# Kernel tuning notes

Hardware: AMD Instinct MI355X
Metric: run time of the kernel (lower is better)

## Reference

```python
import jax, jax.numpy as jnp
import numpy as np

INFEATURES = 4096
OUTFEATURES = 11008
GROUP_SIZE = 128
N_GROUPS = INFEATURES // GROUP_SIZE  # 32
PACK = 8  # 32 bits / 4 bits


def _unpack_int4(packed):
    # packed: [R, C//8] int32 -> [R, C] int32 nibbles in [0, 15]
    shifts = (jnp.arange(PACK, dtype=jnp.int32) * 4)
    nib = (packed[:, :, None] >> shifts[None, None, :]) & 0xF
    return nib.reshape(packed.shape[0], packed.shape[1] * PACK)


def setup_inputs() -> dict:
    key = jax.random.key(0)
    k1, k2, k3, k4, k5 = jax.random.split(key, 5)
    x = jax.random.normal(k1, (2048, INFEATURES), dtype=jnp.float32)
    qweight = jax.random.randint(k2, (INFEATURES, OUTFEATURES // PACK), 0, 2147483647, dtype=jnp.int32)
    qzeros = jax.random.randint(k3, (N_GROUPS, OUTFEATURES // PACK), 0, 2147483647, dtype=jnp.int32)
    scales = jax.random.uniform(k4, (N_GROUPS, OUTFEATURES), minval=0.001, maxval=0.01, dtype=jnp.float32)
    bias = jax.random.normal(k5, (OUTFEATURES,), dtype=jnp.float32) * 0.01
    return {"x": x, "qweight": qweight, "qzeros": qzeros, "scales": scales, "bias": bias}


def reference(x, qweight, qzeros, scales, bias):
    # convert_from_uint4: dequantize packed int4 weight with per-group scale/zero
    w_int = _unpack_int4(qweight)                       # [in, out] int4 values
    z_int = _unpack_int4(qzeros)                        # [n_groups, out]
    dt = scales.dtype
    # broadcast group params to per-row (trivial g_idx: row i -> group i // GROUP_SIZE)
    z = jnp.repeat(z_int.astype(dt), GROUP_SIZE, axis=0)      # [in, out]
    s = jnp.repeat(scales, GROUP_SIZE, axis=0)                # [in, out]
    weight = (w_int.astype(dt) - z) * s                       # [in, out]
    out = jnp.matmul(x, weight) + bias                        # [tokens, out]
    return out
```

## Files before the change

kernel.cpp:

```cpp
#include <hip/hip_runtime.h>

typedef __bf16 bf16_t;
typedef bf16_t bf16x8 __attribute__((ext_vector_type(8)));
typedef float  floatx4 __attribute__((ext_vector_type(4)));
typedef unsigned int uint;

constexpr int Mdim = 2048;
constexpr int Kdim = 4096;
constexpr int Ndim = 11008;
constexpr int NPK  = Ndim / 8;
constexpr int BM = 128, BN = 128, BK = 64;
constexpr int SA = 72;
constexpr int SB = 72;
constexpr int SQ = 68;

#define GLOAD_LDS16(g, l) \
    __builtin_amdgcn_global_load_lds((const __attribute__((address_space(1))) void*)(g), \
                                     (__attribute__((address_space(3))) void*)(l), 16, 0, 0)

__global__ void xcast_kernel(const float* __restrict__ x, bf16_t* __restrict__ xb)
{
    const int i = (blockIdx.x * 256 + threadIdx.x) * 8;
    const float4 a = *(const float4*)(x + i);
    const float4 b = *(const float4*)(x + i + 4);
    bf16x8 v;
    v[0] = (bf16_t)a.x; v[1] = (bf16_t)a.y; v[2] = (bf16_t)a.z; v[3] = (bf16_t)a.w;
    v[4] = (bf16_t)b.x; v[5] = (bf16_t)b.y; v[6] = (bf16_t)b.z; v[7] = (bf16_t)b.w;
    *(bf16x8*)(xb + i) = v;
}

__global__ __launch_bounds__(256, 4)
void wdeq_kernel(const uint* __restrict__ qweight, const uint* __restrict__ qzeros,
                 const float* __restrict__ scales, bf16_t* __restrict__ wt)
{
    __shared__ uint qbuf[16 * SQ];
    const int t  = threadIdx.x;
    const int n0 = blockIdx.x * 128;
    const int k0 = blockIdx.y * 64;
    const int c0 = n0 >> 3;
    const int g  = k0 >> 7;

    const int qk  = t >> 2;
    const int qc4 = (t & 3) * 4;
    const uint4 w4 = *(const uint4*)(qweight + (size_t)(k0 + qk) * NPK + c0 + qc4);
    qbuf[(qc4 + 0) * SQ + qk] = w4.x;
    qbuf[(qc4 + 1) * SQ + qk] = w4.y;
    qbuf[(qc4 + 2) * SQ + qk] = w4.z;
    qbuf[(qc4 + 3) * SQ + qk] = w4.w;
    __syncthreads();

    const int nloc  = t & 127;
    const int khalf = t >> 7;
    const int cc    = nloc >> 3;
    const int jsh   = (nloc & 7) * 4;

    const uint  zw = qzeros[(size_t)g * NPK + c0 + cc];
    const float s  = scales[(size_t)g * Ndim + n0 + nloc];
    const float zs = (float)((zw >> jsh) & 15u) * s;
    const uint* qrow = &qbuf[cc * SQ + khalf * 32];
    bf16_t* dst = wt + (size_t)(n0 + nloc) * Kdim + k0 + khalf * 32;
#pragma unroll
    for (int j = 0; j < 4; ++j) {
        const uint4 qa = *(const uint4*)(qrow + j * 8);
        const uint4 qb = *(const uint4*)(qrow + j * 8 + 4);
        bf16x8 v;
        v[0] = (bf16_t)((float)((qa.x >> jsh) & 15u) * s - zs);
        v[1] = (bf16_t)((float)((qa.y >> jsh) & 15u) * s - zs);
        v[2] = (bf16_t)((float)((qa.z >> jsh) & 15u) * s - zs);
        v[3] = (bf16_t)((float)((qa.w >> jsh) & 15u) * s - zs);
        v[4] = (bf16_t)((float)((qb.x >> jsh) & 15u) * s - zs);
        v[5] = (bf16_t)((float)((qb.y >> jsh) & 15u) * s - zs);
        v[6] = (bf16_t)((float)((qb.z >> jsh) & 15u) * s - zs);
        v[7] = (bf16_t)((float)((qb.w >> jsh) & 15u) * s - zs);
        *(bf16x8*)(dst + j * 8) = v;
    }
}

template <bool PREX>
__global__ __launch_bounds__(256, 4)
void gemm_kernel(const float* __restrict__ x, const bf16_t* __restrict__ xb,
                 const bf16_t* __restrict__ wt, const float* __restrict__ bias,
                 float* __restrict__ out)
{
    constexpr int SAg = PREX ? 64 : 72;
    __shared__ bf16_t As[128 * SAg];
    __shared__ bf16_t Bs[128 * 64];

    const int t    = threadIdx.x;
    const int m0   = blockIdx.y * BM;
    const int n0   = blockIdx.x * BN;
    const int wave = t >> 6;
    const int lane = t & 63;
    const int quad = lane >> 4;
    const int l16  = lane & 15;
    const int mw = (wave >> 1) * 64;
    const int nw = (wave & 1) * 64;

    floatx4 acc[4][4];
#pragma unroll
    for (int i = 0; i < 4; ++i)
#pragma unroll
        for (int j = 0; j < 4; ++j)
            acc[i][j] = (floatx4){0.f, 0.f, 0.f, 0.f};

    const int am = t >> 3;
    const int ao = t & 7;
    const int lr = lane >> 3;
    const int lo = (lane & 7) * 8;

    for (int kt = 0; kt < Kdim / BK; ++kt) {
        const int k0 = kt * BK;

        if (PREX) {
#pragma unroll
            for (int p = 0; p < 4; ++p) {
                const int q = wave * 4 + p;
                GLOAD_LDS16(xb + (size_t)(m0 + q * 8 + lr) * Kdim + k0 + lo,
                            As + q * 512);
            }
        } else {
#pragma unroll
            for (int p = 0; p < 4; ++p) {
                const int m = p * 32 + am;
                const float* src = x + (size_t)(m0 + m) * Kdim + k0 + ao * 8;
                const float4 a = *(const float4*)src;
                const float4 b = *(const float4*)(src + 4);
                bf16x8 v;
                v[0] = (bf16_t)a.x; v[1] = (bf16_t)a.y; v[2] = (bf16_t)a.z; v[3] = (bf16_t)a.w;
                v[4] = (bf16_t)b.x; v[5] = (bf16_t)b.y; v[6] = (bf16_t)b.z; v[7] = (bf16_t)b.w;
                *(bf16x8*)&As[m * SAg + ao * 8] = v;
            }
        }
#pragma unroll
        for (int p = 0; p < 4; ++p) {
            const int q = wave * 4 + p;
            GLOAD_LDS16(wt + (size_t)(n0 + q * 8 + lr) * Kdim + k0 + lo,
                        Bs + q * 512);
        }
        __syncthreads();

#pragma unroll
        for (int s = 0; s < 2; ++s) {
            bf16x8 fa[4], fb[4];
#pragma unroll
            for (int mt = 0; mt < 4; ++mt)
                fa[mt] = *(const bf16x8*)&As[(mw + mt * 16 + l16) * SAg + s * 32 + quad * 8];
#pragma unroll
            for (int nt = 0; nt < 4; ++nt)
                fb[nt] = *(const bf16x8*)&Bs[(nw + nt * 16 + l16) * 64 + s * 32 + quad * 8];
#pragma unroll
            for (int mt = 0; mt < 4; ++mt)
#pragma unroll
                for (int nt = 0; nt < 4; ++nt)
                    acc[mt][nt] = __builtin_amdgcn_mfma_f32_16x16x32_bf16(fa[mt], fb[nt], acc[mt][nt], 0, 0, 0);
        }
        __syncthreads();
    }

#pragma unroll
    for (int nt = 0; nt < 4; ++nt) {
        const int col = n0 + nw + nt * 16 + l16;
        const float b = bias[col];
#pragma unroll
        for (int mt = 0; mt < 4; ++mt) {
#pragma unroll
            for (int r = 0; r < 4; ++r) {
                const int row = m0 + mw + mt * 16 + quad * 4 + r;
                out[(size_t)row * Ndim + col] = acc[mt][nt][r] + b;
            }
        }
    }
}

template <bool PRE>
__global__ __launch_bounds__(256, 3)
void qgemm_kernel(const float* __restrict__ x,
                  const bf16_t* __restrict__ xb,
                  const uint* __restrict__ qweight,
                  const uint* __restrict__ qzeros,
                  const float* __restrict__ scales,
                  const float* __restrict__ bias,
                  float* __restrict__ out)
{
    __shared__ bf16_t As[BM * SA];
    __shared__ bf16_t Bs[BN * SB];
    __shared__ uint   qbuf[16 * SQ];

    const int t  = threadIdx.x;
    const int m0 = blockIdx.y * BM;
    const int n0 = blockIdx.x * BN;
    const int c0 = n0 >> 3;

    const int wave = t >> 6;
    const int lane = t & 63;
    const int quad = lane >> 4;
    const int l16  = lane & 15;
    const int mw = (wave >> 1) * 64;
    const int nw = (wave & 1) * 64;

    floatx4 acc[4][4];
#pragma unroll
    for (int i = 0; i < 4; ++i)
#pragma unroll
        for (int j = 0; j < 4; ++j)
            acc[i][j] = (floatx4){0.f, 0.f, 0.f, 0.f};

    const int am = t >> 3;
    const int ao = t & 7;
    const int qk  = t >> 2;
    const int qc4 = (t & 3) * 4;
    const int nloc  = t & 127;
    const int khalf = t >> 7;
    const int cc    = nloc >> 3;
    const int jsh   = (nloc & 7) * 4;

    for (int kt = 0; kt < Kdim / BK; ++kt) {
        const int k0 = kt * BK;
        const int g  = k0 >> 7;

#pragma unroll
        for (int p = 0; p < 4; ++p) {
            const int m = p * 32 + am;
            if (PRE) {
                const bf16x8 v = *(const bf16x8*)(xb + (size_t)(m0 + m) * Kdim + k0 + ao * 8);
                *(bf16x8*)&As[m * SA + ao * 8] = v;
            } else {
                const float* src = x + (size_t)(m0 + m) * Kdim + k0 + ao * 8;
                const float4 a = *(const float4*)src;
                const float4 b = *(const float4*)(src + 4);
                bf16x8 v;
                v[0] = (bf16_t)a.x; v[1] = (bf16_t)a.y; v[2] = (bf16_t)a.z; v[3] = (bf16_t)a.w;
                v[4] = (bf16_t)b.x; v[5] = (bf16_t)b.y; v[6] = (bf16_t)b.z; v[7] = (bf16_t)b.w;
                *(bf16x8*)&As[m * SA + ao * 8] = v;
            }
        }
        {
            const uint4 w4 = *(const uint4*)(qweight + (size_t)(k0 + qk) * NPK + c0 + qc4);
            qbuf[(qc4 + 0) * SQ + qk] = w4.x;
            qbuf[(qc4 + 1) * SQ + qk] = w4.y;
            qbuf[(qc4 + 2) * SQ + qk] = w4.z;
            qbuf[(qc4 + 3) * SQ + qk] = w4.w;
        }
        __syncthreads();

        {
            const uint  zw = qzeros[(size_t)g * NPK + c0 + cc];
            const float s  = scales[(size_t)g * Ndim + n0 + nloc];
            const float zs = (float)((zw >> jsh) & 15u) * s;
            const uint* qrow = &qbuf[cc * SQ + khalf * 32];
#pragma unroll
            for (int j = 0; j < 4; ++j) {
                const uint4 qa = *(const uint4*)(qrow + j * 8);
                const uint4 qb = *(const uint4*)(qrow + j * 8 + 4);
                bf16x8 v;
                v[0] = (bf16_t)((float)((qa.x >> jsh) & 15u) * s - zs);
                v[1] = (bf16_t)((float)((qa.y >> jsh) & 15u) * s - zs);
                v[2] = (bf16_t)((float)((qa.z >> jsh) & 15u) * s - zs);
                v[3] = (bf16_t)((float)((qa.w >> jsh) & 15u) * s - zs);
                v[4] = (bf16_t)((float)((qb.x >> jsh) & 15u) * s - zs);
                v[5] = (bf16_t)((float)((qb.y >> jsh) & 15u) * s - zs);
                v[6] = (bf16_t)((float)((qb.z >> jsh) & 15u) * s - zs);
                v[7] = (bf16_t)((float)((qb.w >> jsh) & 15u) * s - zs);
                *(bf16x8*)&Bs[nloc * SB + khalf * 32 + j * 8] = v;
            }
        }
        __syncthreads();

#pragma unroll
        for (int s = 0; s < 2; ++s) {
            bf16x8 fa[4], fb[4];
#pragma unroll
            for (int mt = 0; mt < 4; ++mt)
                fa[mt] = *(const bf16x8*)&As[(mw + mt * 16 + l16) * SA + s * 32 + quad * 8];
#pragma unroll
            for (int nt = 0; nt < 4; ++nt)
                fb[nt] = *(const bf16x8*)&Bs[(nw + nt * 16 + l16) * SB + s * 32 + quad * 8];
#pragma unroll
            for (int mt = 0; mt < 4; ++mt)
#pragma unroll
                for (int nt = 0; nt < 4; ++nt)
                    acc[mt][nt] = __builtin_amdgcn_mfma_f32_16x16x32_bf16(fa[mt], fb[nt], acc[mt][nt], 0, 0, 0);
        }
        __syncthreads();
    }

#pragma unroll
    for (int nt = 0; nt < 4; ++nt) {
        const int col = n0 + nw + nt * 16 + l16;
        const float b = bias[col];
#pragma unroll
        for (int mt = 0; mt < 4; ++mt) {
#pragma unroll
            for (int r = 0; r < 4; ++r) {
                const int row = m0 + mw + mt * 16 + quad * 4 + r;
                out[(size_t)row * Ndim + col] = acc[mt][nt][r] + b;
            }
        }
    }
}

extern "C" void kernel_launch(void* const* d_in, const int* in_sizes, int n_in,
                              void* d_out, int out_size, void* d_ws, size_t ws_size,
                              hipStream_t stream)
{
    const float* x        = (const float*)d_in[0];
    const uint*  qweight  = (const uint*)d_in[1];
    const uint*  qzeros   = (const uint*)d_in[2];
    const float* scales   = (const float*)d_in[3];
    const float* bias     = (const float*)d_in[4];
    float*       out      = (float*)d_out;

    const size_t wb_bytes = (size_t)Kdim * Ndim * sizeof(bf16_t);
    const size_t xb_bytes = (size_t)Mdim * Kdim * sizeof(bf16_t);

    dim3 ggrid(Ndim / BN, Mdim / BM);

    if (ws_size >= wb_bytes) {
        bf16_t* wt = (bf16_t*)d_ws;
        wdeq_kernel<<<dim3(Ndim / 128, Kdim / 64), 256, 0, stream>>>(qweight, qzeros, scales, wt);
        if (ws_size >= wb_bytes + xb_bytes) {
            bf16_t* xb = (bf16_t*)((char*)d_ws + wb_bytes);
            xcast_kernel<<<(Mdim * Kdim) / (256 * 8), 256, 0, stream>>>(x, xb);
            gemm_kernel<true><<<ggrid, dim3(256), 0, stream>>>(x, xb, wt, bias, out);
        } else {
            gemm_kernel<false><<<ggrid, dim3(256), 0, stream>>>(x, nullptr, wt, bias, out);
        }
    } else {
        bf16_t* xb = (bf16_t*)d_ws;
        if (ws_size >= xb_bytes) {
            xcast_kernel<<<(Mdim * Kdim) / (256 * 8), 256, 0, stream>>>(x, xb);
            qgemm_kernel<true><<<ggrid, dim3(256), 0, stream>>>(x, xb, qweight, qzeros, scales, bias, out);
        } else {
            qgemm_kernel<false><<<ggrid, dim3(256), 0, stream>>>(x, xb, qweight, qzeros, scales, bias, out);
        }
    }
}
```

Measured before the change: 409.8 us.

## Replace bf16 GEMM with 256x128 double-buffered 8-wave kernel with swizzled LDS

Replaces the 128x128 single-buffered GEMM with a 512-thread kernel computing 256x128 tiles. It double-buffers LDS, prefetches the next K tiles via global_load_lds interleaved with MFMA using explicit waitcnt, barriers and setprio, XOR-swizzles LDS to avoid bank conflicts, and remaps block indices for L2 locality. The goal is to hide global load latency and raise MFMA utilisation. The price is larger LDS use, lower occupancy and hand-tuned wait counts that could be fragile. The old gemm fallback without a cached x cast is dropped.

```diff
diff --git a/kernel.cpp b/kernel.cpp
--- a/kernel.cpp
+++ b/kernel.cpp
@@ -9,14 +9,20 @@
 constexpr int Kdim = 4096;
 constexpr int Ndim = 11008;
 constexpr int NPK  = Ndim / 8;
+constexpr int SQ   = 68;
 constexpr int BM = 128, BN = 128, BK = 64;
-constexpr int SA = 72;
-constexpr int SB = 72;
-constexpr int SQ = 68;
+constexpr int SA = 72, SB = 72;
 
 #define GLOAD_LDS16(g, l) \
     __builtin_amdgcn_global_load_lds((const __attribute__((address_space(1))) void*)(g), \
                                      (__attribute__((address_space(3))) void*)(l), 16, 0, 0)
+#define MFMA(a, b, c) __builtin_amdgcn_mfma_f32_16x16x32_bf16((a), (b), (c), 0, 0, 0)
+#define BAR()    __builtin_amdgcn_s_barrier()
+#define LGKM0()  asm volatile("s_waitcnt lgkmcnt(0)" ::: "memory")
+#define LGKM8()  asm volatile("s_waitcnt lgkmcnt(8)" ::: "memory")
+#define VMCNT2() asm volatile("s_waitcnt vmcnt(2)" ::: "memory")
+#define PRIO1()  __builtin_amdgcn_s_setprio(1)
+#define PRIO0()  __builtin_amdgcn_s_setprio(0)
 
 __global__ void xcast_kernel(const float* __restrict__ x, bf16_t* __restrict__ xb)
 {
@@ -76,97 +82,135 @@
     }
 }
 
-template <bool PREX>
-__global__ __launch_bounds__(256, 4)
-void gemm_kernel(const float* __restrict__ x, const bf16_t* __restrict__ xb,
-                 const bf16_t* __restrict__ wt, const float* __restrict__ bias,
-                 float* __restrict__ out)
-{
-    constexpr int SAg = PREX ? 64 : 72;
-    __shared__ bf16_t As[128 * SAg];
-    __shared__ bf16_t Bs[128 * 64];
+__global__ __launch_bounds__(512, 2)
+void gemm8_kernel(const bf16_t* __restrict__ xb, const bf16_t* __restrict__ wt,
+                  const float* __restrict__ bias, float* __restrict__ out)
+{
+    __shared__ bf16_t As[2 * 16384];
+    __shared__ bf16_t Bs[2 * 8192];
 
     const int t    = threadIdx.x;
-    const int m0   = blockIdx.y * BM;
-    const int n0   = blockIdx.x * BN;
-    const int wave = t >> 6;
+    const int w    = t >> 6;
     const int lane = t & 63;
     const int quad = lane >> 4;
     const int l16  = lane & 15;
-    const int mw = (wave >> 1) * 64;
-    const int nw = (wave & 1) * 64;
-
-    floatx4 acc[4][4];
-#pragma unroll
-    for (int i = 0; i < 4; ++i)
-#pragma unroll
-        for (int j = 0; j < 4; ++j)
+    const int wm   = w >> 2;
+    const int wn   = w & 3;
+    const int w64  = w * 64;
+
+    const int flat = blockIdx.y * 86 + blockIdx.x;
+    const int nf   = (flat & 7) * 86 + (flat >> 3);
+    const int m0   = (nf / 86) * 256;
+    const int n0   = (nf % 86) * 128;
+
+    auto stageA = [&](int T, int h) {
+        const int p  = T & 1;
+        const int Tk = (T & 63) * 64;
+#pragma unroll
+        for (int l = 0; l < 2; ++l) {
+            const int idx = l * 512 + w64 + lane;
+            const int r   = idx >> 3;
+            const int bc  = (idx & 7) ^ (r & 7);
+            GLOAD_LDS16(xb + (size_t)(m0 + h * 128 + r) * Kdim + Tk + bc * 8,
+                        As + (p * 16384 + h * 8192 + (l * 512 + w64) * 8));
+        }
+    };
+    auto stageB = [&](int T) {
+        const int p  = T & 1;
+        const int Tk = (T & 63) * 64;
+#pragma unroll
+        for (int l = 0; l < 2; ++l) {
+            const int idx = l * 512 + w64 + lane;
+            const int r   = idx >> 3;
+            const int bc  = (idx & 7) ^ (r & 7);
+            GLOAD_LDS16(wt + (size_t)(n0 + r) * Kdim + Tk + bc * 8,
+                        Bs + (p * 8192 + (l * 512 + w64) * 8));
+        }
+    };
+    auto lda = [&](int p, int mt, int s) -> bf16x8 {
+        const int r = mt * 16 + l16;
+        return *(const bf16x8*)(As + p * 16384 + wm * 8192 + r * 64 +
+                                ((s * 4 + quad) ^ (l16 & 7)) * 8);
+    };
+    auto ldb = [&](int p, int nt, int s) -> bf16x8 {
+        const int r = wn * 32 + nt * 16 + l16;
+        return *(const bf16x8*)(Bs + p * 8192 + r * 64 +
+                                ((s * 4 + quad) ^ (l16 & 7)) * 8);
+    };
+
+    floatx4 acc[8][2];
+#pragma unroll
+    for (int i = 0; i < 8; ++i)
+#pragma unroll
+        for (int j = 0; j < 2; ++j)
             acc[i][j] = (floatx4){0.f, 0.f, 0.f, 0.f};
 
-    const int am = t >> 3;
-    const int ao = t & 7;
-    const int lr = lane >> 3;
-    const int lo = (lane & 7) * 8;
-
-    for (int kt = 0; kt < Kdim / BK; ++kt) {
-        const int k0 = kt * BK;
-
-        if (PREX) {
-#pragma unroll
-            for (int p = 0; p < 4; ++p) {
-                const int q = wave * 4 + p;
-                GLOAD_LDS16(xb + (size_t)(m0 + q * 8 + lr) * Kdim + k0 + lo,
-                            As + q * 512);
-            }
-        } else {
-#pragma unroll
-            for (int p = 0; p < 4; ++p) {
-                const int m = p * 32 + am;
-                const float* src = x + (size_t)(m0 + m) * Kdim + k0 + ao * 8;
-                const float4 a = *(const float4*)src;
-                const float4 b = *(const float4*)(src + 4);
-                bf16x8 v;
-                v[0] = (bf16_t)a.x; v[1] = (bf16_t)a.y; v[2] = (bf16_t)a.z; v[3] = (bf16_t)a.w;
-                v[4] = (bf16_t)b.x; v[5] = (bf16_t)b.y; v[6] = (bf16_t)b.z; v[7] = (bf16_t)b.w;
-                *(bf16x8*)&As[m * SAg + ao * 8] = v;
-            }
-        }
-#pragma unroll
-        for (int p = 0; p < 4; ++p) {
-            const int q = wave * 4 + p;
-            GLOAD_LDS16(wt + (size_t)(n0 + q * 8 + lr) * Kdim + k0 + lo,
-                        Bs + q * 512);
-        }
-        __syncthreads();
-
-#pragma unroll
-        for (int s = 0; s < 2; ++s) {
-            bf16x8 fa[4], fb[4];
-#pragma unroll
-            for (int mt = 0; mt < 4; ++mt)
-                fa[mt] = *(const bf16x8*)&As[(mw + mt * 16 + l16) * SAg + s * 32 + quad * 8];
-#pragma unroll
-            for (int nt = 0; nt < 4; ++nt)
-                fb[nt] = *(const bf16x8*)&Bs[(nw + nt * 16 + l16) * 64 + s * 32 + quad * 8];
-#pragma unroll
-            for (int mt = 0; mt < 4; ++mt)
-#pragma unroll
-                for (int nt = 0; nt < 4; ++nt)
-                    acc[mt][nt] = __builtin_amdgcn_mfma_f32_16x16x32_bf16(fa[mt], fb[nt], acc[mt][nt], 0, 0, 0);
-        }
-        __syncthreads();
-    }
-
-#pragma unroll
-    for (int nt = 0; nt < 4; ++nt) {
-        const int col = n0 + nw + nt * 16 + l16;
-        const float b = bias[col];
-#pragma unroll
-        for (int mt = 0; mt < 4; ++mt) {
+    stageA(0, 0); stageA(0, 1); stageB(0); stageB(1);
+    VMCNT2(); BAR();
+
+    bf16x8 av0[4], av1[4], bb[4];
+
+#define MFMA16(MG)                                                         \
+    PRIO1();                                                               \
+    _Pragma("unroll") for (int mt = 0; mt < 4; ++mt) {                     \
+        acc[(MG)*4 + mt][0] = MFMA(av0[mt], bb[0], acc[(MG)*4 + mt][0]);   \
+        acc[(MG)*4 + mt][1] = MFMA(av0[mt], bb[1], acc[(MG)*4 + mt][1]);   \
+    }                                                                      \
+    _Pragma("unroll") for (int mt = 0; mt < 4; ++mt) {                     \
+        acc[(MG)*4 + mt][0] = MFMA(av1[mt], bb[2], acc[(MG)*4 + mt][0]);   \
+        acc[(MG)*4 + mt][1] = MFMA(av1[mt], bb[3], acc[(MG)*4 + mt][1]);   \
+    }                                                                      \
+    PRIO0();
+
+    for (int i = 0; i < 32; ++i) {
+        bb[0] = ldb(0, 0, 0); bb[1] = ldb(0, 1, 0);
+        bb[2] = ldb(0, 0, 1); bb[3] = ldb(0, 1, 1);
+#pragma unroll
+        for (int mt = 0; mt < 4; ++mt) { av0[mt] = lda(0, mt, 0); av1[mt] = lda(0, mt, 1); }
+        stageA(2 * i + 1, 0); stageA(2 * i + 1, 1);
+        LGKM8();
+        BAR(); LGKM0();
+        MFMA16(0);
+        BAR();
+
+#pragma unroll
+        for (int mt = 0; mt < 4; ++mt) { av0[mt] = lda(0, mt + 4, 0); av1[mt] = lda(0, mt + 4, 1); }
+        stageB(2 * i + 2);
+        VMCNT2();
+        BAR(); LGKM0();
+        MFMA16(1);
+        BAR();
+
+        bb[0] = ldb(1, 0, 0); bb[1] = ldb(1, 1, 0);
+        bb[2] = ldb(1, 0, 1); bb[3] = ldb(1, 1, 1);
+#pragma unroll
+        for (int mt = 0; mt < 4; ++mt) { av0[mt] = lda(1, mt, 0); av1[mt] = lda(1, mt, 1); }
+        stageA(2 * i + 2, 0); stageA(2 * i + 2, 1);
+        LGKM8();
+        BAR(); LGKM0();
+        MFMA16(0);
+        BAR();
+
+#pragma unroll
+        for (int mt = 0; mt < 4; ++mt) { av0[mt] = lda(1, mt + 4, 0); av1[mt] = lda(1, mt + 4, 1); }
+        stageB(2 * i + 3);
+        VMCNT2();
+        BAR(); LGKM0();
+        MFMA16(1);
+        BAR();
+    }
+#undef MFMA16
+
+#pragma unroll
+    for (int nt = 0; nt < 2; ++nt) {
+        const int col = n0 + wn * 32 + nt * 16 + l16;
+        const float bv = bias[col];
+#pragma unroll
+        for (int mt = 0; mt < 8; ++mt) {
 #pragma unroll
             for (int r = 0; r < 4; ++r) {
-                const int row = m0 + mw + mt * 16 + quad * 4 + r;
-                out[(size_t)row * Ndim + col] = acc[mt][nt][r] + b;
+                const int row = m0 + wm * 128 + mt * 16 + quad * 4 + r;
+                out[(size_t)row * Ndim + col] = acc[mt][nt][r] + bv;
             }
         }
     }
@@ -279,7 +323,7 @@
             for (int mt = 0; mt < 4; ++mt)
 #pragma unroll
                 for (int nt = 0; nt < 4; ++nt)
-                    acc[mt][nt] = __builtin_amdgcn_mfma_f32_16x16x32_bf16(fa[mt], fb[nt], acc[mt][nt], 0, 0, 0);
+                    acc[mt][nt] = MFMA(fa[mt], fb[nt], acc[mt][nt]);
         }
         __syncthreads();
     }
@@ -313,25 +357,20 @@
     const size_t wb_bytes = (size_t)Kdim * Ndim * sizeof(bf16_t);
     const size_t xb_bytes = (size_t)Mdim * Kdim * sizeof(bf16_t);
 
-    dim3 ggrid(Ndim / BN, Mdim / BM);
-
-    if (ws_size >= wb_bytes) {
+    if (ws_size >= wb_bytes + xb_bytes) {
         bf16_t* wt = (bf16_t*)d_ws;
+        bf16_t* xbuf = (bf16_t*)((char*)d_ws + wb_bytes);
         wdeq_kernel<<<dim3(Ndim / 128, Kdim / 64), 256, 0, stream>>>(qweight, qzeros, scales, wt);
-        if (ws_size >= wb_bytes + xb_bytes) {
-            bf16_t* xb = (bf16_t*)((char*)d_ws + wb_bytes);
-            xcast_kernel<<<(Mdim * Kdim) / (256 * 8), 256, 0, stream>>>(x, xb);
-            gemm_kernel<true><<<ggrid, dim3(256), 0, stream>>>(x, xb, wt, bias, out);
+        xcast_kernel<<<(Mdim * Kdim) / (256 * 8), 256, 0, stream>>>(x, xbuf);
+        gemm8_kernel<<<dim3(86, 8), dim3(512), 0, stream>>>(xbuf, wt, bias, out);
+    } else {
+        bf16_t* xbuf = (bf16_t*)d_ws;
+        dim3 ggrid(Ndim / BN, Mdim / BM);
+        if (ws_size >= xb_bytes) {
+            xcast_kernel<<<(Mdim * Kdim) / (256 * 8), 256, 0, stream>>>(x, xbuf);
+            qgemm_kernel<true><<<ggrid, dim3(256), 0, stream>>>(x, xbuf, qweight, qzeros, scales, bias, out);
         } else {
-            gemm_kernel<false><<<ggrid, dim3(256), 0, stream>>>(x, nullptr, wt, bias, out);
-        }
-    } else {
-        bf16_t* xb = (bf16_t*)d_ws;
-        if (ws_size >= xb_bytes) {
-            xcast_kernel<<<(Mdim * Kdim) / (256 * 8), 256, 0, stream>>>(x, xb);
-            qgemm_kernel<true><<<ggrid, dim3(256), 0, stream>>>(x, xb, qweight, qzeros, scales, bias, out);
-        } else {
-            qgemm_kernel<false><<<ggrid, dim3(256), 0, stream>>>(x, xb, qweight, qzeros, scales, bias, out);
-        }
-    }
-}
+            qgemm_kernel<false><<<ggrid, dim3(256), 0, stream>>>(x, xbuf, qweight, qzeros, scales, bias, out);
+        }
+    }
+}
```

New measurement: 394.1 us. 1.04x faster.
